# Kernel tuning notes

Measured on AMD Instinct MI355X. Metric: run time of the kernel, lower is better.

Reference implementation:

```python
import jax, jax.numpy as jnp
import numpy as np

B, T, E, H, A, V, C = 4, 256, 256, 256, 256, 32000, 100
NEG = -1e9


def setup_inputs() -> dict:
    key = jax.random.key(0)
    cnt = [0]
    def nk():
        cnt[0] += 1
        return jax.random.fold_in(key, cnt[0])
    def rn(shape, scale=0.05):
        return jax.random.normal(nk(), shape, jnp.float32) * scale
    inp = {
        'input_ids': jax.random.randint(nk(), (B, T), 0, V),
        'category_ids': jax.random.randint(nk(), (B, T), 0, C),
        'emb': rn((V, E)),
        'cat_emb': rn((C, E)),
    }
    in_sizes = [2 * E, H]
    for li, ins in enumerate(in_sizes):
        inp[f'Wih{li}'] = rn((ins, 3 * H)); inp[f'bih{li}'] = rn((3 * H,))
        inp[f'Whh{li}'] = rn((H, 3 * H)); inp[f'bhh{li}'] = rn((3 * H,))
        inp[f'Wh{li}'] = rn((H, A));      inp[f'bh{li}'] = rn((A,))
        inp[f'Wx{li}'] = rn((ins, A));    inp[f'bx{li}'] = rn((A,))
        inp[f'Wth{li}'] = rn((H, A));     inp[f'bth{li}'] = rn((A,))
        inp[f'v{li}'] = rn((A,));         inp[f'bv{li}'] = rn((1,))
    inp['Wctx'] = rn((H + E, 500)); inp['bctx'] = rn((500,))
    inp['Wout'] = rn((500, V));     inp['bout'] = rn((V,))
    return inp


def _cell(x, h, tape, t, Wih, bih, Whh, bhh, Wh, bh, Wx, bx, Wth, bth, v, bv):
    # attention over memory tape positions j < t (tape rows >= t are zeros, masked out)
    att = jnp.tanh(tape @ Wh + bh + (x @ Wx + bx)[:, None, :] + (h @ Wth + bth)[:, None, :])  # [B,T,A]
    scores = att @ v + bv  # [B,T]
    mask = jnp.arange(tape.shape[1]) < t
    scores = jnp.where(mask[None, :], scores, NEG)
    w = jax.nn.softmax(scores, axis=1)
    agg = jnp.einsum('bt,bth->bh', w, tape)
    agg = jnp.where(t > 0, agg, h)  # empty tape at t=0 -> use hidden directly
    gi = x @ Wih + bih
    gh = agg @ Whh + bhh
    ir, iu, inew = jnp.split(gi, 3, axis=1)
    hr, hu, hn = jnp.split(gh, 3, axis=1)
    r = jax.nn.sigmoid(ir + hr)
    u = jax.nn.sigmoid(iu + hu)
    n = jnp.tanh(inew + r * hn)
    return (1.0 - u) * n + u * agg


def _forward(input_ids, category_ids, emb, cat_emb, p0, p1, Wctx, bctx, Wout, bout):
    we = emb[input_ids]          # [B,T,E]
    ce = cat_emb[category_ids]   # [B,T,E]
    x_seq = jnp.concatenate([we, ce], axis=-1)  # [B,T,2E]

    def step(carry, xs):
        h0, h1, tape0, tape1 = carry
        x_t, c_t, t = xs
        # layer 0: category added to both embedding halves
        li0 = jax.nn.relu(x_t + jnp.tile(c_t, (1, 2)))
        nh0 = _cell(li0, h0, tape0, t, *p0)
        tape0 = tape0.at[:, t].set(nh0)
        # layer 1 (dropout is identity in eval)
        li1 = jax.nn.relu(nh0 + c_t)
        nh1 = _cell(li1, h1, tape1, t, *p1)
        tape1 = tape1.at[:, t].set(nh1)
        ctx = jnp.tanh(jnp.concatenate([nh1, c_t], axis=-1) @ Wctx + bctx)
        logits = ctx @ Wout + bout
        return (nh0, nh1, tape0, tape1), logits

    Bn = input_ids.shape[0]
    init = (jnp.zeros((Bn, H), jnp.float32), jnp.zeros((Bn, H), jnp.float32),
            jnp.zeros((Bn, T, H), jnp.float32), jnp.zeros((Bn, T, H), jnp.float32))
    xs = (jnp.swapaxes(x_seq, 0, 1), jnp.swapaxes(ce, 0, 1), jnp.arange(T))
    (h0, h1, _, _), outs = jax.lax.scan(jax.checkpoint(step), init, xs)
    return jnp.swapaxes(outs, 0, 1), h0, h1


def reference(input_ids, category_ids, emb, cat_emb,
              Wih0, bih0, Whh0, bhh0, Wh0, bh0, Wx0, bx0, Wth0, bth0, v0, bv0,
              Wih1, bih1, Whh1, bhh1, Wh1, bh1, Wx1, bx1, Wth1, bth1, v1, bv1,
              Wctx, bctx, Wout, bout):
    p0 = (Wih0, bih0, Whh0, bhh0, Wh0, bh0, Wx0, bx0, Wth0, bth0, v0, bv0)
    p1 = (Wih1, bih1, Whh1, bhh1, Wh1, bh1, Wx1, bx1, Wth1, bth1, v1, bv1)
    return _forward(input_ids, category_ids, emb, cat_emb, p0, p1, Wctx, bctx, Wout, bout)
```

## Files before the change

### kernel.cpp

```cpp
#include <hip/hip_runtime.h>

#define DEVINL __device__ __forceinline__

constexpr int kB = 4, kT = 256, kH = 256, kA = 256, kV = 32000;
constexpr int NBLK = 64;
constexpr int NGRP = 32;
constexpr int NTHR = 512;
constexpr int WSL = 8;
constexpr int SBIAS = 1 << 24;
constexpr int SBIAS_TOT = NGRP * SBIAS;
constexpr unsigned long long CANARY = ~0ull;

typedef __attribute__((ext_vector_type(8))) short bf16x8;
typedef __attribute__((ext_vector_type(4))) float f32x4;

DEVINL float fexp2(float x) { float y; asm("v_exp_f32 %0, %1" : "=v"(y) : "v"(x)); return y; }
DEVINL float frcp(float x)  { float y; asm("v_rcp_f32 %0, %1" : "=v"(y) : "v"(x)); return y; }
DEVINL float f_tanh(float x) {
  float t = fexp2(x * 2.88539008f);
  return 1.f - 2.f * frcp(t + 1.f);
}
DEVINL float f_sig(float x) { return frcp(1.f + fexp2(-x * 1.44269504f)); }

DEVINL float bfu2f(unsigned short u) {
  union { unsigned int i; float f; } c; c.i = ((unsigned int)u) << 16; return c.f;
}
DEVINL unsigned short f2bfu(float f) {
  union { float f; unsigned int i; } c; c.f = f;
  unsigned int r = c.i + 0x7fffu + ((c.i >> 16) & 1u);
  return (unsigned short)(r >> 16);
}
DEVINL unsigned int f2u(float f) { union { float f; unsigned int i; } c; c.f = f; return c.i; }
DEVINL float u2f(unsigned int u) { union { unsigned int i; float f; } c; c.i = u; return c.f; }

DEVINL unsigned long long aload64(const unsigned long long* p) {
  return __hip_atomic_load(p, __ATOMIC_RELAXED, __HIP_MEMORY_SCOPE_AGENT);
}
DEVINL void astore64(unsigned long long* p, unsigned long long v) {
  __hip_atomic_store(p, v, __ATOMIC_RELAXED, __HIP_MEMORY_SCOPE_AGENT);
}

DEVINL bool sready(unsigned long long v) {
  unsigned int lo = (unsigned int)v, hi = (unsigned int)(v >> 32);
  return (((lo + (1u << 23)) >> 24) == (unsigned)NGRP) &&
         (((hi + (1u << 23)) >> 24) == (unsigned)NGRP);
}

DEVINL float dot_bf128(const float* x, const unsigned short* w) {
  float a0 = 0.f, a1 = 0.f, a2 = 0.f, a3 = 0.f;
  float a4 = 0.f, a5 = 0.f, a6 = 0.f, a7 = 0.f;
  const float4*  x4 = (const float4*)x;
  const ushort4* w4 = (const ushort4*)w;
#pragma unroll
  for (int i = 0; i < 32; i += 2) {
    float4 xv0 = x4[i], xv1 = x4[i + 1];
    ushort4 wv0 = w4[i], wv1 = w4[i + 1];
    a0 += xv0.x * bfu2f(wv0.x);
    a1 += xv0.y * bfu2f(wv0.y);
    a2 += xv0.z * bfu2f(wv0.z);
    a3 += xv0.w * bfu2f(wv0.w);
    a4 += xv1.x * bfu2f(wv1.x);
    a5 += xv1.y * bfu2f(wv1.y);
    a6 += xv1.z * bfu2f(wv1.z);
    a7 += xv1.w * bfu2f(wv1.w);
  }
  return ((a0 + a1) + (a2 + a3)) + ((a4 + a5) + (a6 + a7));
}

DEVINL float sc4(const unsigned short* p4p, const float* xp, const float* vr) {
  ushort4 p4 = *(const ushort4*)p4p;
  float accA, accB;
  accA  = f_tanh(bfu2f(p4.x) + xp[0]) * vr[0];
  accB  = f_tanh(bfu2f(p4.y) + xp[1]) * vr[1];
  accA += f_tanh(bfu2f(p4.z) + xp[2]) * vr[2];
  accB += f_tanh(bfu2f(p4.w) + xp[3]) * vr[3];
  return accA + accB;
}

__global__ void init_kernel(int* dst, int nz, int val) {
  for (int i = blockIdx.x * blockDim.x + threadIdx.x; i < nz; i += gridDim.x * blockDim.x)
    dst[i] = val;
}

__global__ void embed_kernel(const int* __restrict__ ids, const int* __restrict__ cids,
                             const float* __restrict__ emb, const float* __restrict__ cat_emb,
                             float* __restrict__ li0_all, float* __restrict__ ce_all,
                             float* __restrict__ cat1_all) {
  int bt = blockIdx.x, e = threadIdx.x;
  int id = ids[bt], cid = cids[bt];
  float we = emb[id * kH + e];
  float ce = cat_emb[cid * kH + e];
  li0_all[bt * 512 + e]       = fmaxf(we + ce, 0.f);
  li0_all[bt * 512 + 256 + e] = fmaxf(ce + ce, 0.f);
  ce_all[bt * 256 + e] = ce;
  cat1_all[bt * 512 + 256 + e] = ce;
}

__global__ __launch_bounds__(256) void gemm_f32(const float* __restrict__ A,
                                                const float* __restrict__ Wm,
                                                const float* __restrict__ bias,
                                                float* __restrict__ C,
                                                int M, int N, int K) {
  __shared__ __align__(16) float As[16][68];
  __shared__ __align__(16) float Bs[16][68];
  int tid = threadIdx.x;
  int tx = tid & 15, ty = tid >> 4;
  int row0 = blockIdx.y * 64, col0 = blockIdx.x * 64;
  int ar = tid >> 2;
  int ak = (tid & 3) * 4;
  int br = tid >> 4;
  int bc = (tid & 15) * 4;
  float acc[4][4] = {};
  for (int k0 = 0; k0 < K; k0 += 16) {
    float4 av = {0.f, 0.f, 0.f, 0.f};
    if (k0 + ak < K) av = *(const float4*)(A + (size_t)(row0 + ar) * K + k0 + ak);
    As[ak + 0][ar] = av.x; As[ak + 1][ar] = av.y; As[ak + 2][ar] = av.z; As[ak + 3][ar] = av.w;
    float4 bv = {0.f, 0.f, 0.f, 0.f};
    int wrow = k0 + br;
    if (wrow < K) {
      if (col0 + bc + 3 < N) bv = *(const float4*)(Wm + (size_t)wrow * N + col0 + bc);
      else {
        float t[4] = {0.f, 0.f, 0.f, 0.f};
        for (int u = 0; u < 4; ++u) if (col0 + bc + u < N) t[u] = Wm[(size_t)wrow * N + col0 + bc + u];
        bv.x = t[0]; bv.y = t[1]; bv.z = t[2]; bv.w = t[3];
      }
    }
    *(float4*)&Bs[br][bc] = bv;
    __syncthreads();
#pragma unroll
    for (int kk = 0; kk < 16; ++kk) {
      float4 a4 = *(const float4*)&As[kk][ty * 4];
      float4 b4 = *(const float4*)&Bs[kk][tx * 4];
      acc[0][0] += a4.x * b4.x; acc[0][1] += a4.x * b4.y; acc[0][2] += a4.x * b4.z; acc[0][3] += a4.x * b4.w;
      acc[1][0] += a4.y * b4.x; acc[1][1] += a4.y * b4.y; acc[1][2] += a4.y * b4.z; acc[1][3] += a4.y * b4.w;
      acc[2][0] += a4.z * b4.x; acc[2][1] += a4.z * b4.y; acc[2][2] += a4.z * b4.z; acc[2][3] += a4.z * b4.w;
      acc[3][0] += a4.w * b4.x; acc[3][1] += a4.w * b4.y; acc[3][2] += a4.w * b4.z; acc[3][3] += a4.w * b4.w;
    }
    __syncthreads();
  }
#pragma unroll
  for (int i = 0; i < 4; ++i) {
    int r = row0 + ty * 4 + i;
#pragma unroll
    for (int j = 0; j < 4; ++j) {
      int c = col0 + tx * 4 + j;
      if (c < N) C[(size_t)r * N + c] = acc[i][j] + bias[c];
    }
  }
}

__global__ __launch_bounds__(256) void gemm_ctx_bf16(const float* __restrict__ A,
                                                     const float* __restrict__ Wm,
                                                     const float* __restrict__ bias,
                                                     unsigned short* __restrict__ Cb) {
  const int N = 500, K = 512;
  __shared__ __align__(16) float As[16][68];
  __shared__ __align__(16) float Bs[16][68];
  int tid = threadIdx.x;
  int tx = tid & 15, ty = tid >> 4;
  int row0 = blockIdx.y * 64, col0 = blockIdx.x * 64;
  int ar = tid >> 2;
  int ak = (tid & 3) * 4;
  int br = tid >> 4;
  int bc = (tid & 15) * 4;
  float acc[4][4] = {};
  for (int k0 = 0; k0 < K; k0 += 16) {
    float4 av = *(const float4*)(A + (size_t)(row0 + ar) * K + k0 + ak);
    As[ak + 0][ar] = av.x; As[ak + 1][ar] = av.y; As[ak + 2][ar] = av.z; As[ak + 3][ar] = av.w;
    float4 bv = {0.f, 0.f, 0.f, 0.f};
    int wrow = k0 + br;
    if (col0 + bc + 3 < N) bv = *(const float4*)(Wm + (size_t)wrow * N + col0 + bc);
    else {
      float t[4] = {0.f, 0.f, 0.f, 0.f};
      for (int u = 0; u < 4; ++u) if (col0 + bc + u < N) t[u] = Wm[(size_t)wrow * N + col0 + bc + u];
      bv.x = t[0]; bv.y = t[1]; bv.z = t[2]; bv.w = t[3];
    }
    *(float4*)&Bs[br][bc] = bv;
    __syncthreads();
#pragma unroll
    for (int kk = 0; kk < 16; ++kk) {
      float4 a4 = *(const float4*)&As[kk][ty * 4];
      float4 b4 = *(const float4*)&Bs[kk][tx * 4];
      acc[0][0] += a4.x * b4.x; acc[0][1] += a4.x * b4.y; acc[0][2] += a4.x * b4.z; acc[0][3] += a4.x * b4.w;
      acc[1][0] += a4.y * b4.x; acc[1][1] += a4.y * b4.y; acc[1][2] += a4.y * b4.z; acc[1][3] += a4.y * b4.w;
      acc[2][0] += a4.z * b4.x; acc[2][1] += a4.z * b4.y; acc[2][2] += a4.z * b4.z; acc[2][3] += a4.z * b4.w;
      acc[3][0] += a4.w * b4.x; acc[3][1] += a4.w * b4.y; acc[3][2] += a4.w * b4.z; acc[3][3] += a4.w * b4.w;
    }
    __syncthreads();
  }
#pragma unroll
  for (int i = 0; i < 4; ++i) {
    int r = row0 + ty * 4 + i;
#pragma unroll
    for (int j = 0; j < 4; ++j) {
      int c = col0 + tx * 4 + j;
      if (c < N) {
        float v = f_tanh(acc[i][j] + bias[c]);
        Cb[(size_t)r * 512 + c] = f2bfu(v);
      } else {
        Cb[(size_t)r * 512 + c] = 0;
      }
    }
  }
}

__global__ __launch_bounds__(256) void gemm_logits_mfma(
    const unsigned short* __restrict__ A,
    const float* __restrict__ Wout,
    const float* __restrict__ bout,
    float* __restrict__ C) {
  __shared__ __align__(16) unsigned short Bt[64][520];
  const int tid = threadIdx.x;
  const int n0 = blockIdx.x * 64;

  for (int idx = tid; idx < 512 * 16; idx += 256) {
    int k = idx >> 4, nq = (idx & 15) << 2;
    if (k < 500) {
      float4 v = *(const float4*)(Wout + (size_t)k * 32000 + n0 + nq);
      Bt[nq + 0][k] = f2bfu(v.x); Bt[nq + 1][k] = f2bfu(v.y);
      Bt[nq + 2][k] = f2bfu(v.z); Bt[nq + 3][k] = f2bfu(v.w);
    } else {
      Bt[nq + 0][k] = 0; Bt[nq + 1][k] = 0; Bt[nq + 2][k] = 0; Bt[nq + 3][k] = 0;
    }
  }
  __syncthreads();

  const int l = tid & 63, w = tid >> 6;
  const int lrow = l & 15, lk = (l >> 4) * 8;
  float bia0 = bout[n0 +  0 + lrow];
  float bia1 = bout[n0 + 16 + lrow];
  float bia2 = bout[n0 + 32 + lrow];
  float bia3 = bout[n0 + 48 + lrow];

  for (int m0 = 0; m0 < 1024; m0 += 64) {
    f32x4 acc0 = {0.f, 0.f, 0.f, 0.f}, acc1 = acc0, acc2 = acc0, acc3 = acc0;
    const unsigned short* Arow = A + (size_t)(m0 + w * 16 + lrow) * 512 + lk;
#pragma unroll
    for (int ks = 0; ks < 16; ++ks) {
      bf16x8 a  = *(const bf16x8*)(Arow + ks * 32);
      bf16x8 b0 = *(const bf16x8*)&Bt[ 0 + lrow][ks * 32 + lk];
      bf16x8 b1 = *(const bf16x8*)&Bt[16 + lrow][ks * 32 + lk];
      bf16x8 b2 = *(const bf16x8*)&Bt[32 + lrow][ks * 32 + lk];
      bf16x8 b3 = *(const bf16x8*)&Bt[48 + lrow][ks * 32 + lk];
      acc0 = __builtin_amdgcn_mfma_f32_16x16x32_bf16(a, b0, acc0, 0, 0, 0);
      acc1 = __builtin_amdgcn_mfma_f32_16x16x32_bf16(a, b1, acc1, 0, 0, 0);
      acc2 = __builtin_amdgcn_mfma_f32_16x16x32_bf16(a, b2, acc2, 0, 0, 0);
      acc3 = __builtin_amdgcn_mfma_f32_16x16x32_bf16(a, b3, acc3, 0, 0, 0);
    }
    int orow = m0 + w * 16 + (l >> 4) * 4;
#pragma unroll
    for (int r = 0; r < 4; ++r) {
      float* Cr = C + (size_t)(orow + r) * 32000 + n0;
      Cr[ 0 + lrow] = acc0[r] + bia0;
      Cr[16 + lrow] = acc1[r] + bia1;
      Cr[32 + lrow] = acc2[r] + bia2;
      Cr[48 + lrow] = acc3[r] + bia3;
    }
  }
}

__global__ __launch_bounds__(NTHR, 1) void coop_kernel(
    const float* __restrict__ gi0_all, const float* __restrict__ xw0_all,
    const float* __restrict__ ce_all,
    unsigned long long* __restrict__ nh0p, unsigned long long* __restrict__ nh1p,
    float* __restrict__ cat1_all, float* __restrict__ out_tail,
    unsigned long long* __restrict__ s0buf, unsigned long long* __restrict__ s1buf,
    const float* __restrict__ Whh0, const float* __restrict__ bhh0,
    const float* __restrict__ Wh0, const float* __restrict__ bh0,
    const float* __restrict__ Wth0, const float* __restrict__ bth0,
    const float* __restrict__ v0,
    const float* __restrict__ Wih1, const float* __restrict__ bih1,
    const float* __restrict__ Whh1, const float* __restrict__ bhh1,
    const float* __restrict__ Wh1, const float* __restrict__ bh1,
    const float* __restrict__ Wx1, const float* __restrict__ bx1,
    const float* __restrict__ Wth1, const float* __restrict__ bth1,
    const float* __restrict__ v1) {
  __shared__ __align__(16) unsigned short tWhh0_s[kT][24][2];
  __shared__ __align__(16) unsigned short tWhh1_s[kT][24][2];
  __shared__ __align__(16) unsigned short tape0_s[kT][16];
  __shared__ __align__(16) unsigned short tape1_s[kT][16];
  __shared__ __align__(16) unsigned short tWh0_s[2][kT][8];
  __shared__ __align__(16) unsigned short tWh1_s[2][kT][8];
  __shared__ __align__(16) unsigned short Wh0c[WSL][264], Wth0c[WSL][264];
  __shared__ __align__(16) unsigned short Wh1c[WSL][264], Wth1c[WSL][264], Wx1c[WSL][264];
  __shared__ __align__(16) unsigned short Whh0c[24][264], Whh1c[24][264], Wih1c[24][264];
  __shared__ float bh0s[8], bth0s[8], bh1s[8], bth1s[8], bx1s[8];
  __shared__ float bhh0s[24], bhh1s[24], bih1s[24];
  __shared__ __align__(16) float nh0_s[2][260], nh1_s[2][260], li1_s[2][260];
  __shared__ __align__(16) float sm_s[4][260];
  __shared__ float xps0_s[2][8], xps1a_s[2][8], xps1b_s[2][8];
  __shared__ float gi1_s[2][24], gh0_s[2][24], gh1_s[2][24];
  __shared__ float agg0_s[2][8], agg1_s[2][8], redsum_s[4][2];
  __shared__ float gipre_s[2][3][8];
  __shared__ float v0s[8], v1s[8];

  const int bid = blockIdx.x, tid = threadIdx.x;
  const int grp = bid >> 5;
  const int bidg = bid & 31;
  const int c0 = bidg * WSL;
  unsigned long long* S0 = s0buf + grp * 768;
  unsigned long long* S1 = s1buf + grp * 768;

  for (int idx = tid; idx < WSL * kH; idx += NTHR) {
    int c = idx >> 8, h = idx & 255, col = c0 + c;
    Wh0c[c][h]  = f2bfu(Wh0[h * kA + col]);
    Wth0c[c][h] = f2bfu(Wth0[h * kA + col]);
    Wh1c[c][h]  = f2bfu(Wh1[h * kA + col]);
    Wth1c[c][h] = f2bfu(Wth1[h * kA + col]);
    Wx1c[c][h]  = f2bfu(Wx1[h * kA + col]);
  }
  for (int idx = tid; idx < 24 * kH; idx += NTHR) {
    int cc = idx >> 8, h = idx & 255;
    int n = (cc >> 3) * kH + c0 + (cc & 7);
    Whh0c[cc][h] = f2bfu(Whh0[h * 768 + n]);
    Whh1c[cc][h] = f2bfu(Whh1[h * 768 + n]);
    Wih1c[cc][h] = f2bfu(Wih1[h * 768 + n]);
  }
  if (tid < 8) {
    int c = c0 + tid;
    bh0s[tid] = bh0[c]; bth0s[tid] = bth0[c];
    bh1s[tid] = bh1[c]; bth1s[tid] = bth1[c]; bx1s[tid] = bx1[c];
    v0s[tid] = v0[c]; v1s[tid] = v1[c];
  }
  if (tid < 24) {
    int n = (tid >> 3) * kH + c0 + (tid & 7);
    bhh0s[tid] = bhh0[n]; bhh1s[tid] = bhh1[n]; bih1s[tid] = bih1[n];
  }
  __syncthreads();

  if (tid < 16) {
    int b = tid & 1, c = tid >> 1, gb = grp * 2 + b;
    const float* gi = gi0_all + (size_t)(gb * kT) * 768;
    int hcol = c0 + c;
    float r = f_sig(gi[hcol] + bhh0s[c]);
    float u = f_sig(gi[256 + hcol] + bhh0s[8 + c]);
    float n = f_tanh(gi[512 + hcol] + r * bhh0s[16 + c]);
    float val = (1.f - u) * n;
    tape0_s[0][c * 2 + b] = f2bfu(val);
    float other = __shfl_xor(val, 2);
    if ((c & 1) == 0) {
      unsigned long long pk = (unsigned long long)f2u(val) |
                              ((unsigned long long)f2u(other) << 32);
      astore64(&nh0p[(size_t)(gb * kT) * 128 + bidg * 4 + (c >> 1)], pk);
    }
  }

  const float SCL = 65536.f;
  const float fxi = 1.44269504f / 65536.f;

  for (int k = 0; k < kT; ++k) {
    {
      int which = tid >> 8;
      int slot = tid & 255;
      int b = slot >> 7, pr = slot & 127, h = pr * 2, gb = grp * 2 + b;
      if (which == 0) {
        const unsigned long long* p = &nh0p[(size_t)(gb * kT + k) * 128 + pr];
        unsigned long long v = aload64(p);
        int it = 0;
        while (v == CANARY) {
          v = aload64(p);
          if (++it > (1 << 24)) break;
        }
        float lo = u2f((unsigned int)v), hi = u2f((unsigned int)(v >> 32));
        nh0_s[b][h] = lo; nh0_s[b][h + 1] = hi;
        float2 ce2 = *(const float2*)&ce_all[(size_t)(gb * kT + k) * 256 + h];
        li1_s[b][h]     = fmaxf(lo + ce2.x, 0.f);
        li1_s[b][h + 1] = fmaxf(hi + ce2.y, 0.f);
      } else if (k > 0) {
        const unsigned long long* p = &nh1p[(size_t)(gb * kT + k - 1) * 128 + pr];
        unsigned long long v = aload64(p);
        int it = 0;
        while (v == CANARY) {
          v = aload64(p);
          if (++it > (1 << 24)) break;
        }
        nh1_s[b][h]     = u2f((unsigned int)v);
        nh1_s[b][h + 1] = u2f((unsigned int)(v >> 32));
      }
    }
    if (tid < 16 && k < kT - 1) {
      int b = tid & 1, c = tid >> 1, gb = grp * 2 + b, hcol = c0 + c;
      const float* gi = gi0_all + (size_t)(gb * kT + k + 1) * 768;
      gipre_s[b][0][c] = gi[hcol];
      gipre_s[b][1][c] = gi[256 + hcol];
      gipre_s[b][2][c] = gi[512 + hcol];
    }
    if (tid >= NTHR - 16) {
      int z = tid - (NTHR - 16);
      int pz = (k + 1) % 3;
      int idx = bidg * 8 + (z & 7);
      if (z < 8) astore64(&S0[pz * 256 + idx], 0ull);
      else       astore64(&S1[pz * 256 + idx], 0ull);
    }
    __syncthreads();

    {
      int p = tid >> 1, half = tid & 1, off = half * 128;
      if (p < 80) {
        if (k < kT - 1) {
          if (p < 16) {
            int b = p & 1, c = p >> 1, gb = grp * 2 + b;
            float xw = xw0_all[(size_t)(gb * kT + k + 1) * kA + c0 + c];
            float acc = dot_bf128(nh0_s[b] + off, Wth0c[c] + off);
            acc += __shfl_xor(acc, 1);
            if (half == 0) xps0_s[b][c] = acc + bth0s[c] + xw;
          } else if (p < 32) {
            int s2 = p - 16; int b = s2 & 1, c = s2 >> 1;
            float acc = dot_bf128(nh0_s[b] + off, Wh0c[c] + off);
            acc += __shfl_xor(acc, 1);
            if (half == 0) tWh0_s[b][k][c] = f2bfu(acc + bh0s[c]);
          } else {
            int s2 = p - 32; int b = s2 & 1, cc = s2 >> 1;
            float acc = dot_bf128(nh0_s[b] + off, Whh0c[cc] + off);
            acc += __shfl_xor(acc, 1);
            if (half == 0) tWhh0_s[k][cc][b] = f2bfu(acc);
          }
        }
      } else if (p < 144) {
        if (p < 96) {
          int s2 = p - 80; int b = s2 & 1, c = s2 >> 1;
          float acc = dot_bf128(li1_s[b] + off, Wx1c[c] + off);
          acc += __shfl_xor(acc, 1);
          if (half == 0) xps1a_s[b][c] = acc + bx1s[c];
        } else {
          int s3 = p - 96; int b = s3 & 1, cc = s3 >> 1;
          float acc = dot_bf128(li1_s[b] + off, Wih1c[cc] + off);
          acc += __shfl_xor(acc, 1);
          if (half == 0) gi1_s[b][cc] = acc + bih1s[cc];
        }
      } else if (p < 224) {
        if (k > 0) {
          if (p < 160) {
            int s2 = p - 144; int b = s2 & 1, c = s2 >> 1;
            float acc = dot_bf128(nh1_s[b] + off, Wth1c[c] + off);
            acc += __shfl_xor(acc, 1);
            if (half == 0) xps1b_s[b][c] = acc + bth1s[c];
          } else if (p < 176) {
            int s3 = p - 160; int b = s3 & 1, c = s3 >> 1;
            float acc = dot_bf128(nh1_s[b] + off, Wh1c[c] + off);
            acc += __shfl_xor(acc, 1);
            if (half == 0) tWh1_s[b][k - 1][c] = f2bfu(acc + bh1s[c]);
          } else {
            int s3 = p - 176; int b = s3 & 1, cc = s3 >> 1;
            float acc = dot_bf128(nh1_s[b] + off, Whh1c[cc] + off);
            acc += __shfl_xor(acc, 1);
            if (half == 0) tWhh1_s[k - 1][cc][b] = f2bfu(acc);
          }
        }
      }
    }
    __syncthreads();

    {
      int cnt0w = k + 1, cnt1w = k;
      int np0 = (k < kT - 1) ? ((cnt0w + 1) >> 1) * 2 : 0;
      int np1 = ((cnt1w + 1) >> 1) * 2;
      int pk = k % 3;
      unsigned long long* d0 = S0 + pk * 256;
      unsigned long long* d1 = S1 + pk * 256;
      for (int pp = tid; pp < np0 + np1; pp += NTHR) {
        float p0, p1; unsigned long long* dst;
        if (pp < np0) {
          int pr = pp >> 1, b = pp & 1, j0 = 2 * pr;
          const float* xp = &xps0_s[b][0];
          p0 = sc4(&tWh0_s[b][j0][0], xp, v0s) + sc4(&tWh0_s[b][j0][4], xp + 4, v0s + 4);
          p1 = 0.f;
          if (j0 + 1 < cnt0w)
            p1 = sc4(&tWh0_s[b][j0 + 1][0], xp, v0s) + sc4(&tWh0_s[b][j0 + 1][4], xp + 4, v0s + 4);
          dst = d0 + b * 128 + pr;
        } else {
          int q = pp - np0; int pr = q >> 1, b = q & 1, j0 = 2 * pr;
          float xp[8];
#pragma unroll
          for (int c = 0; c < 8; ++c) xp[c] = xps1a_s[b][c] + xps1b_s[b][c];
          p0 = sc4(&tWh1_s[b][j0][0], xp, v1s) + sc4(&tWh1_s[b][j0][4], xp + 4, v1s + 4);
          p1 = 0.f;
          if (j0 + 1 < cnt1w)
            p1 = sc4(&tWh1_s[b][j0 + 1][0], xp, v1s) + sc4(&tWh1_s[b][j0 + 1][4], xp + 4, v1s + 4);
          dst = d1 + b * 128 + pr;
        }
        int q0 = (int)rintf(p0 * SCL) + SBIAS;
        int q1 = (int)rintf(p1 * SCL) + SBIAS;
        unsigned long long add = (unsigned long long)(unsigned int)q0 |
                                 ((unsigned long long)(unsigned int)q1 << 32);
        __hip_atomic_fetch_add(dst, add, __ATOMIC_RELAXED, __HIP_MEMORY_SCOPE_AGENT);
      }
    }
    __syncthreads();

    int cnt0 = (k < kT - 1) ? (k + 1) : 0;
    int cnt1 = k;
    {
      int r = tid >> 7, lane = tid & 127;
      float sum = 0.f;
      int cnt = (r < 2) ? cnt0 : cnt1;
      if (cnt) {
        int pk = k % 3;
        const unsigned long long* sb = (r < 2)
            ? S0 + pk * 256 + (r & 1) * 128
            : S1 + pk * 256 + (r & 1) * 128;
        int npr = (cnt + 1) >> 1;
        if (lane < npr) {
          unsigned long long v = aload64(&sb[lane]);
          int it = 0;
          while (!sready(v)) {
            v = aload64(&sb[lane]);
            if (++it > (1 << 24)) break;
          }
          int lo = (int)(unsigned int)(v & 0xffffffffull) - SBIAS_TOT;
          int hi = (int)(unsigned int)(v >> 32) - SBIAS_TOT;
          float e0 = fexp2((float)lo * fxi);
          sm_s[r][2 * lane] = e0; sum += e0;
          if (2 * lane + 1 < cnt) {
            float e1 = fexp2((float)hi * fxi);
            sm_s[r][2 * lane + 1] = e1; sum += e1;
          }
        }
      }
      for (int m = 32; m >= 1; m >>= 1) sum += __shfl_xor(sum, m);
      if ((tid & 63) == 0) redsum_s[r][(tid >> 6) & 1] = sum;
    }
    __syncthreads();

    {
      int slot = tid >> 2, sub = tid & 3;
      float accA = 0.f, accB = 0.f;
      if (slot < 48) {
        if (cnt0) {
          int b = slot & 1, cc = slot >> 1;
#pragma unroll 4
          for (int j = sub; j < cnt0; j += 8) accA += sm_s[b][j] * bfu2f(tWhh0_s[j][cc][b]);
#pragma unroll 4
          for (int j = sub + 4; j < cnt0; j += 8) accB += sm_s[b][j] * bfu2f(tWhh0_s[j][cc][b]);
          float acc = accA + accB;
          acc += __shfl_xor(acc, 1); acc += __shfl_xor(acc, 2);
          if (sub == 0) gh0_s[b][cc] = acc * frcp(redsum_s[b][0] + redsum_s[b][1]) + bhh0s[cc];
        }
      } else if (slot < 64) {
        if (cnt0) {
          int s2 = slot - 48; int b = s2 & 1, c = s2 >> 1;
#pragma unroll 4
          for (int j = sub; j < cnt0; j += 8) accA += sm_s[b][j] * bfu2f(tape0_s[j][c * 2 + b]);
#pragma unroll 4
          for (int j = sub + 4; j < cnt0; j += 8) accB += sm_s[b][j] * bfu2f(tape0_s[j][c * 2 + b]);
          float acc = accA + accB;
          acc += __shfl_xor(acc, 1); acc += __shfl_xor(acc, 2);
          if (sub == 0) agg0_s[b][c] = acc * frcp(redsum_s[b][0] + redsum_s[b][1]);
        }
      } else if (slot < 112) {
        if (cnt1) {
          int s2 = slot - 64; int b = s2 & 1, cc = s2 >> 1;
#pragma unroll 4
          for (int j = sub; j < cnt1; j += 8) accA += sm_s[2 + b][j] * bfu2f(tWhh1_s[j][cc][b]);
#pragma unroll 4
          for (int j = sub + 4; j < cnt1; j += 8) accB += sm_s[2 + b][j] * bfu2f(tWhh1_s[j][cc][b]);
          float acc = accA + accB;
          acc += __shfl_xor(acc, 1); acc += __shfl_xor(acc, 2);
          if (sub == 0) gh1_s[b][cc] = acc * frcp(redsum_s[2 + b][0] + redsum_s[2 + b][1]) + bhh1s[cc];
        }
      } else if (slot < 128) {
        if (cnt1) {
          int s2 = slot - 112; int b = s2 & 1, c = s2 >> 1;
#pragma unroll 4
          for (int j = sub; j < cnt1; j += 8) accA += sm_s[2 + b][j] * bfu2f(tape1_s[j][c * 2 + b]);
#pragma unroll 4
          for (int j = sub + 4; j < cnt1; j += 8) accB += sm_s[2 + b][j] * bfu2f(tape1_s[j][c * 2 + b]);
          float acc = accA + accB;
          acc += __shfl_xor(acc, 1); acc += __shfl_xor(acc, 2);
          if (sub == 0) agg1_s[b][c] = acc * frcp(redsum_s[2 + b][0] + redsum_s[2 + b][1]);
        }
      }
    }
    __syncthreads();

    if (tid < 16) {
      if (k < kT - 1) {
        int b = tid & 1, c = tid >> 1, gb = grp * 2 + b, hcol = c0 + c, t0 = k + 1;
        float agg = agg0_s[b][c];
        float r = f_sig(gipre_s[b][0][c] + gh0_s[b][c]);
        float u = f_sig(gipre_s[b][1][c] + gh0_s[b][8 + c]);
        float n = f_tanh(gipre_s[b][2][c] + r * gh0_s[b][16 + c]);
        float val = (1.f - u) * n + u * agg;
        tape0_s[t0][c * 2 + b] = f2bfu(val);
        if (t0 == kT - 1) out_tail[gb * kH + hcol] = val;
        float other = __shfl_xor(val, 2);
        if ((c & 1) == 0) {
          unsigned long long pk = (unsigned long long)f2u(val) |
                                  ((unsigned long long)f2u(other) << 32);
          astore64(&nh0p[(size_t)(gb * kT + t0) * 128 + bidg * 4 + (c >> 1)], pk);
        }
      }
    } else if (tid >= 64 && tid < 80) {
      int t2 = tid - 64; int b = t2 & 1, c = t2 >> 1, gb = grp * 2 + b, hcol = c0 + c;
      float ghr, ghu, ghn, agg;
      if (k > 0) { ghr = gh1_s[b][c]; ghu = gh1_s[b][8 + c]; ghn = gh1_s[b][16 + c]; agg = agg1_s[b][c]; }
      else       { ghr = bhh1s[c];    ghu = bhh1s[8 + c];    ghn = bhh1s[16 + c];    agg = 0.f; }
      float r = f_sig(gi1_s[b][c] + ghr);
      float u = f_sig(gi1_s[b][8 + c] + ghu);
      float n = f_tanh(gi1_s[b][16 + c] + r * ghn);
      float val = (1.f - u) * n + u * agg;
      tape1_s[k][c * 2 + b] = f2bfu(val);
      cat1_all[(size_t)(gb * kT + k) * 512 + hcol] = val;
      if (k == kT - 1) out_tail[kB * kH + gb * kH + hcol] = val;
      float other = __shfl_xor(val, 2);
      if ((c & 1) == 0) {
        unsigned long long pk = (unsigned long long)f2u(val) |
                                ((unsigned long long)f2u(other) << 32);
        astore64(&nh1p[(size_t)(gb * kT + k) * 128 + bidg * 4 + (c >> 1)], pk);
      }
    }
  }
}

extern "C" void kernel_launch(void* const* d_in, const int* in_sizes, int n_in,
                              void* d_out, int out_size, void* d_ws, size_t ws_size,
                              hipStream_t stream) {
  const int*   input_ids    = (const int*)d_in[0];
  const int*   category_ids = (const int*)d_in[1];
  const float* emb     = (const float*)d_in[2];
  const float* cat_emb = (const float*)d_in[3];
  const float* Wih0 = (const float*)d_in[4];
  const float* bih0 = (const float*)d_in[5];
  const float* Whh0 = (const float*)d_in[6];  const float* bhh0 = (const float*)d_in[7];
  const float* Wh0  = (const float*)d_in[8];  const float* bh0  = (const float*)d_in[9];
  const float* Wx0  = (const float*)d_in[10]; const float* bx0  = (const float*)d_in[11];
  const float* Wth0 = (const float*)d_in[12]; const float* bth0 = (const float*)d_in[13];
  const float* v0   = (const float*)d_in[14];
  const float* Wih1 = (const float*)d_in[16]; const float* bih1 = (const float*)d_in[17];
  const float* Whh1 = (const float*)d_in[18]; const float* bhh1 = (const float*)d_in[19];
  const float* Wh1  = (const float*)d_in[20]; const float* bh1  = (const float*)d_in[21];
  const float* Wx1  = (const float*)d_in[22]; const float* bx1  = (const float*)d_in[23];
  const float* Wth1 = (const float*)d_in[24]; const float* bth1 = (const float*)d_in[25];
  const float* v1   = (const float*)d_in[26];
  const float* Wctx = (const float*)d_in[28]; const float* bctx = (const float*)d_in[29];
  const float* Wout = (const float*)d_in[30]; const float* bout = (const float*)d_in[31];

  float* ws = (float*)d_ws;
  float* li0_all  = ws;
  float* ce_all   = li0_all + 524288;
  float* gi0_all  = ce_all + 262144;
  float* xw0_all  = gi0_all + 786432;
  unsigned long long* nh0p = (unsigned long long*)(xw0_all + 262144);
  unsigned long long* nh1p = nh0p + 131072;
  float* cat1_all = (float*)(nh1p + 131072);
  unsigned short* ctx_bf = (unsigned short*)(cat1_all + 524288);

  unsigned long long* s0buf = (unsigned long long*)li0_all;
  unsigned long long* s1buf = s0buf + 1536;
  int    nzero_s  = 2 * 1536 * 2;
  int    nfill_nh = 2 * 131072 * 2;

  float* out = (float*)d_out;
  float* out_tail = out + (size_t)kB * kT * kV;

  embed_kernel<<<dim3(kB * kT), dim3(256), 0, stream>>>(input_ids, category_ids, emb, cat_emb,
                                                        li0_all, ce_all, cat1_all);
  gemm_f32<<<dim3(12, 16), dim3(256), 0, stream>>>(li0_all, Wih0, bih0, gi0_all, 1024, 768, 512);
  gemm_f32<<<dim3(4, 16), dim3(256), 0, stream>>>(li0_all, Wx0, bx0, xw0_all, 1024, 256, 512);
  init_kernel<<<dim3(8), dim3(512), 0, stream>>>((int*)s0buf, nzero_s, 0);
  init_kernel<<<dim3(128), dim3(512), 0, stream>>>((int*)nh0p, nfill_nh, -1);
  coop_kernel<<<dim3(NBLK), dim3(NTHR), 0, stream>>>(gi0_all, xw0_all, ce_all, nh0p, nh1p,
      cat1_all, out_tail, s0buf, s1buf,
      Whh0, bhh0, Wh0, bh0, Wth0, bth0, v0,
      Wih1, bih1, Whh1, bhh1, Wh1, bh1, Wx1, bx1, Wth1, bth1, v1);
  gemm_ctx_bf16<<<dim3(8, 16), dim3(256), 0, stream>>>(cat1_all, Wctx, bctx, ctx_bf);
  gemm_logits_mfma<<<dim3(500), dim3(256), 0, stream>>>(ctx_bf, Wout, bout, out);
}
```

Before: 2.461 ms.

## Split coop kernel per batch element across 128 blocks instead of 64

Each cooperative block now handles a single batch element instead of two, so the grid doubles to 128 blocks (4 groups of 32). Per-block shared buffers, dot products, the score scratch buffers and the reductions lose their batch dimension. Dot products are split four ways per output with an extra shuffle, and the weighted-sum loops use eight lanes. This shortens the serial per-step critical path inside each block, at the cost of more blocks polling the cross-block sync and each block loading the same weight slices.

Result: faster. 2.072 ms (-15.8%).

```diff
diff --git a/kernel.cpp b/kernel.cpp
--- a/kernel.cpp
+++ b/kernel.cpp
@@ -3,7 +3,7 @@
 #define DEVINL __device__ __forceinline__
 
 constexpr int kB = 4, kT = 256, kH = 256, kA = 256, kV = 32000;
-constexpr int NBLK = 64;
+constexpr int NBLKS = 128;
 constexpr int NGRP = 32;
 constexpr int NTHR = 512;
 constexpr int WSL = 8;
@@ -46,25 +46,19 @@
          (((hi + (1u << 23)) >> 24) == (unsigned)NGRP);
 }
 
-DEVINL float dot_bf128(const float* x, const unsigned short* w) {
+DEVINL float dot_bf64(const float* x, const unsigned short* w) {
   float a0 = 0.f, a1 = 0.f, a2 = 0.f, a3 = 0.f;
-  float a4 = 0.f, a5 = 0.f, a6 = 0.f, a7 = 0.f;
   const float4*  x4 = (const float4*)x;
   const ushort4* w4 = (const ushort4*)w;
 #pragma unroll
-  for (int i = 0; i < 32; i += 2) {
-    float4 xv0 = x4[i], xv1 = x4[i + 1];
-    ushort4 wv0 = w4[i], wv1 = w4[i + 1];
-    a0 += xv0.x * bfu2f(wv0.x);
-    a1 += xv0.y * bfu2f(wv0.y);
-    a2 += xv0.z * bfu2f(wv0.z);
-    a3 += xv0.w * bfu2f(wv0.w);
-    a4 += xv1.x * bfu2f(wv1.x);
-    a5 += xv1.y * bfu2f(wv1.y);
-    a6 += xv1.z * bfu2f(wv1.z);
-    a7 += xv1.w * bfu2f(wv1.w);
-  }
-  return ((a0 + a1) + (a2 + a3)) + ((a4 + a5) + (a6 + a7));
+  for (int i = 0; i < 16; ++i) {
+    float4 xv = x4[i]; ushort4 wv = w4[i];
+    a0 += xv.x * bfu2f(wv.x);
+    a1 += xv.y * bfu2f(wv.y);
+    a2 += xv.z * bfu2f(wv.z);
+    a3 += xv.w * bfu2f(wv.w);
+  }
+  return (a0 + a1) + (a2 + a3);
 }
 
 DEVINL float sc4(const unsigned short* p4p, const float* xp, const float* vr) {
@@ -275,31 +269,32 @@
     const float* __restrict__ Wx1, const float* __restrict__ bx1,
     const float* __restrict__ Wth1, const float* __restrict__ bth1,
     const float* __restrict__ v1) {
-  __shared__ __align__(16) unsigned short tWhh0_s[kT][24][2];
-  __shared__ __align__(16) unsigned short tWhh1_s[kT][24][2];
-  __shared__ __align__(16) unsigned short tape0_s[kT][16];
-  __shared__ __align__(16) unsigned short tape1_s[kT][16];
-  __shared__ __align__(16) unsigned short tWh0_s[2][kT][8];
-  __shared__ __align__(16) unsigned short tWh1_s[2][kT][8];
+  __shared__ __align__(16) unsigned short tWhh0_s[kT][24];
+  __shared__ __align__(16) unsigned short tWhh1_s[kT][24];
+  __shared__ __align__(16) unsigned short tape0_s[kT][8];
+  __shared__ __align__(16) unsigned short tape1_s[kT][8];
+  __shared__ __align__(16) unsigned short tWh0_s[kT][8];
+  __shared__ __align__(16) unsigned short tWh1_s[kT][8];
   __shared__ __align__(16) unsigned short Wh0c[WSL][264], Wth0c[WSL][264];
   __shared__ __align__(16) unsigned short Wh1c[WSL][264], Wth1c[WSL][264], Wx1c[WSL][264];
   __shared__ __align__(16) unsigned short Whh0c[24][264], Whh1c[24][264], Wih1c[24][264];
   __shared__ float bh0s[8], bth0s[8], bh1s[8], bth1s[8], bx1s[8];
   __shared__ float bhh0s[24], bhh1s[24], bih1s[24];
-  __shared__ __align__(16) float nh0_s[2][260], nh1_s[2][260], li1_s[2][260];
-  __shared__ __align__(16) float sm_s[4][260];
-  __shared__ float xps0_s[2][8], xps1a_s[2][8], xps1b_s[2][8];
-  __shared__ float gi1_s[2][24], gh0_s[2][24], gh1_s[2][24];
-  __shared__ float agg0_s[2][8], agg1_s[2][8], redsum_s[4][2];
-  __shared__ float gipre_s[2][3][8];
+  __shared__ __align__(16) float nh0_s[260], nh1_s[260], li1_s[260];
+  __shared__ __align__(16) float sm_s[2][260];
+  __shared__ float xps0_s[8], xps1a_s[8], xps1b_s[8];
+  __shared__ float gi1_s[24], gh0_s[24], gh1_s[24];
+  __shared__ float agg0_s[8], agg1_s[8], redsum_s[2][2];
+  __shared__ float gipre_s[3][8];
   __shared__ float v0s[8], v1s[8];
 
   const int bid = blockIdx.x, tid = threadIdx.x;
   const int grp = bid >> 5;
   const int bidg = bid & 31;
   const int c0 = bidg * WSL;
-  unsigned long long* S0 = s0buf + grp * 768;
-  unsigned long long* S1 = s1buf + grp * 768;
+  const int gb = grp;
+  unsigned long long* S0 = s0buf + grp * 384;
+  unsigned long long* S1 = s1buf + grp * 384;
 
   for (int idx = tid; idx < WSL * kH; idx += NTHR) {
     int c = idx >> 8, h = idx & 255, col = c0 + c;
@@ -328,16 +323,15 @@
   }
   __syncthreads();
 
-  if (tid < 16) {
-    int b = tid & 1, c = tid >> 1, gb = grp * 2 + b;
+  if (tid < 8) {
+    int c = tid, hcol = c0 + c;
     const float* gi = gi0_all + (size_t)(gb * kT) * 768;
-    int hcol = c0 + c;
     float r = f_sig(gi[hcol] + bhh0s[c]);
     float u = f_sig(gi[256 + hcol] + bhh0s[8 + c]);
     float n = f_tanh(gi[512 + hcol] + r * bhh0s[16 + c]);
     float val = (1.f - u) * n;
-    tape0_s[0][c * 2 + b] = f2bfu(val);
-    float other = __shfl_xor(val, 2);
+    tape0_s[0][c] = f2bfu(val);
+    float other = __shfl_xor(val, 1);
     if ((c & 1) == 0) {
       unsigned long long pk = (unsigned long long)f2u(val) |
                               ((unsigned long long)f2u(other) << 32);
@@ -349,10 +343,9 @@
   const float fxi = 1.44269504f / 65536.f;
 
   for (int k = 0; k < kT; ++k) {
-    {
-      int which = tid >> 8;
-      int slot = tid & 255;
-      int b = slot >> 7, pr = slot & 127, h = pr * 2, gb = grp * 2 + b;
+    if (tid < 256) {
+      int which = tid >> 7;
+      int pr = tid & 127, h = pr * 2;
       if (which == 0) {
         const unsigned long long* p = &nh0p[(size_t)(gb * kT + k) * 128 + pr];
         unsigned long long v = aload64(p);
@@ -362,10 +355,10 @@
           if (++it > (1 << 24)) break;
         }
         float lo = u2f((unsigned int)v), hi = u2f((unsigned int)(v >> 32));
-        nh0_s[b][h] = lo; nh0_s[b][h + 1] = hi;
+        nh0_s[h] = lo; nh0_s[h + 1] = hi;
         float2 ce2 = *(const float2*)&ce_all[(size_t)(gb * kT + k) * 256 + h];
-        li1_s[b][h]     = fmaxf(lo + ce2.x, 0.f);
-        li1_s[b][h + 1] = fmaxf(hi + ce2.y, 0.f);
+        li1_s[h]     = fmaxf(lo + ce2.x, 0.f);
+        li1_s[h + 1] = fmaxf(hi + ce2.y, 0.f);
       } else if (k > 0) {
         const unsigned long long* p = &nh1p[(size_t)(gb * kT + k - 1) * 128 + pr];
         unsigned long long v = aload64(p);
@@ -374,77 +367,79 @@
           v = aload64(p);
           if (++it > (1 << 24)) break;
         }
-        nh1_s[b][h]     = u2f((unsigned int)v);
-        nh1_s[b][h + 1] = u2f((unsigned int)(v >> 32));
-      }
-    }
-    if (tid < 16 && k < kT - 1) {
-      int b = tid & 1, c = tid >> 1, gb = grp * 2 + b, hcol = c0 + c;
+        nh1_s[h]     = u2f((unsigned int)v);
+        nh1_s[h + 1] = u2f((unsigned int)(v >> 32));
+      }
+    }
+    if (tid >= 256 && tid < 264 && k < kT - 1) {
+      int c = tid - 256, hcol = c0 + c;
       const float* gi = gi0_all + (size_t)(gb * kT + k + 1) * 768;
-      gipre_s[b][0][c] = gi[hcol];
-      gipre_s[b][1][c] = gi[256 + hcol];
-      gipre_s[b][2][c] = gi[512 + hcol];
-    }
-    if (tid >= NTHR - 16) {
-      int z = tid - (NTHR - 16);
+      gipre_s[0][c] = gi[hcol];
+      gipre_s[1][c] = gi[256 + hcol];
+      gipre_s[2][c] = gi[512 + hcol];
+    }
+    if (tid >= NTHR - 8) {
+      int z = tid - (NTHR - 8);
       int pz = (k + 1) % 3;
-      int idx = bidg * 8 + (z & 7);
-      if (z < 8) astore64(&S0[pz * 256 + idx], 0ull);
-      else       astore64(&S1[pz * 256 + idx], 0ull);
+      int idx = bidg * 4 + (z & 3);
+      if (z < 4) astore64(&S0[pz * 128 + idx], 0ull);
+      else       astore64(&S1[pz * 128 + idx], 0ull);
     }
     __syncthreads();
 
     {
-      int p = tid >> 1, half = tid & 1, off = half * 128;
-      if (p < 80) {
+      int p = tid >> 2, q = tid & 3, off = q * 64;
+      if (p < 40) {
         if (k < kT - 1) {
-          if (p < 16) {
-            int b = p & 1, c = p >> 1, gb = grp * 2 + b;
-            float xw = xw0_all[(size_t)(gb * kT + k + 1) * kA + c0 + c];
-            float acc = dot_bf128(nh0_s[b] + off, Wth0c[c] + off);
-            acc += __shfl_xor(acc, 1);
-            if (half == 0) xps0_s[b][c] = acc + bth0s[c] + xw;
-          } else if (p < 32) {
-            int s2 = p - 16; int b = s2 & 1, c = s2 >> 1;
-            float acc = dot_bf128(nh0_s[b] + off, Wh0c[c] + off);
-            acc += __shfl_xor(acc, 1);
-            if (half == 0) tWh0_s[b][k][c] = f2bfu(acc + bh0s[c]);
+          if (p < 8) {
+            int c = p;
+            float acc = dot_bf64(nh0_s + off, Wth0c[c] + off);
+            acc += __shfl_xor(acc, 1); acc += __shfl_xor(acc, 2);
+            if (q == 0) {
+              float xw = xw0_all[(size_t)(gb * kT + k + 1) * kA + c0 + c];
+              xps0_s[c] = acc + bth0s[c] + xw;
+            }
+          } else if (p < 16) {
+            int c = p - 8;
+            float acc = dot_bf64(nh0_s + off, Wh0c[c] + off);
+            acc += __shfl_xor(acc, 1); acc += __shfl_xor(acc, 2);
+            if (q == 0) tWh0_s[k][c] = f2bfu(acc + bh0s[c]);
           } else {
-            int s2 = p - 32; int b = s2 & 1, cc = s2 >> 1;
-            float acc = dot_bf128(nh0_s[b] + off, Whh0c[cc] + off);
-            acc += __shfl_xor(acc, 1);
-            if (half == 0) tWhh0_s[k][cc][b] = f2bfu(acc);
+            int cc = p - 16;
+            float acc = dot_bf64(nh0_s + off, Whh0c[cc] + off);
+            acc += __shfl_xor(acc, 1); acc += __shfl_xor(acc, 2);
+            if (q == 0) tWhh0_s[k][cc] = f2bfu(acc);
           }
         }
-      } else if (p < 144) {
-        if (p < 96) {
-          int s2 = p - 80; int b = s2 & 1, c = s2 >> 1;
-          float acc = dot_bf128(li1_s[b] + off, Wx1c[c] + off);
-          acc += __shfl_xor(acc, 1);
-          if (half == 0) xps1a_s[b][c] = acc + bx1s[c];
+      } else if (p < 72) {
+        if (p < 64) {
+          int cc = p - 40;
+          float acc = dot_bf64(li1_s + off, Wih1c[cc] + off);
+          acc += __shfl_xor(acc, 1); acc += __shfl_xor(acc, 2);
+          if (q == 0) gi1_s[cc] = acc + bih1s[cc];
         } else {
-          int s3 = p - 96; int b = s3 & 1, cc = s3 >> 1;
-          float acc = dot_bf128(li1_s[b] + off, Wih1c[cc] + off);
-          acc += __shfl_xor(acc, 1);
-          if (half == 0) gi1_s[b][cc] = acc + bih1s[cc];
-        }
-      } else if (p < 224) {
+          int c = p - 64;
+          float acc = dot_bf64(li1_s + off, Wx1c[c] + off);
+          acc += __shfl_xor(acc, 1); acc += __shfl_xor(acc, 2);
+          if (q == 0) xps1a_s[c] = acc + bx1s[c];
+        }
+      } else if (p < 112) {
         if (k > 0) {
-          if (p < 160) {
-            int s2 = p - 144; int b = s2 & 1, c = s2 >> 1;
-            float acc = dot_bf128(nh1_s[b] + off, Wth1c[c] + off);
-            acc += __shfl_xor(acc, 1);
-            if (half == 0) xps1b_s[b][c] = acc + bth1s[c];
-          } else if (p < 176) {
-            int s3 = p - 160; int b = s3 & 1, c = s3 >> 1;
-            float acc = dot_bf128(nh1_s[b] + off, Wh1c[c] + off);
-            acc += __shfl_xor(acc, 1);
-            if (half == 0) tWh1_s[b][k - 1][c] = f2bfu(acc + bh1s[c]);
+          if (p < 80) {
+            int c = p - 72;
+            float acc = dot_bf64(nh1_s + off, Wth1c[c] + off);
+            acc += __shfl_xor(acc, 1); acc += __shfl_xor(acc, 2);
+            if (q == 0) xps1b_s[c] = acc + bth1s[c];
+          } else if (p < 88) {
+            int c = p - 80;
+            float acc = dot_bf64(nh1_s + off, Wh1c[c] + off);
+            acc += __shfl_xor(acc, 1); acc += __shfl_xor(acc, 2);
+            if (q == 0) tWh1_s[k - 1][c] = f2bfu(acc + bh1s[c]);
           } else {
-            int s3 = p - 176; int b = s3 & 1, cc = s3 >> 1;
-            float acc = dot_bf128(nh1_s[b] + off, Whh1c[cc] + off);
-            acc += __shfl_xor(acc, 1);
-            if (half == 0) tWhh1_s[k - 1][cc][b] = f2bfu(acc);
+            int cc = p - 88;
+            float acc = dot_bf64(nh1_s + off, Whh1c[cc] + off);
+            acc += __shfl_xor(acc, 1); acc += __shfl_xor(acc, 2);
+            if (q == 0) tWhh1_s[k - 1][cc] = f2bfu(acc);
           }
         }
       }
@@ -453,31 +448,30 @@
 
     {
       int cnt0w = k + 1, cnt1w = k;
-      int np0 = (k < kT - 1) ? ((cnt0w + 1) >> 1) * 2 : 0;
-      int np1 = ((cnt1w + 1) >> 1) * 2;
+      int np0 = (k < kT - 1) ? ((cnt0w + 1) >> 1) : 0;
+      int np1 = (cnt1w + 1) >> 1;
       int pk = k % 3;
-      unsigned long long* d0 = S0 + pk * 256;
-      unsigned long long* d1 = S1 + pk * 256;
+      unsigned long long* d0 = S0 + pk * 128;
+      unsigned long long* d1 = S1 + pk * 128;
       for (int pp = tid; pp < np0 + np1; pp += NTHR) {
         float p0, p1; unsigned long long* dst;
         if (pp < np0) {
-          int pr = pp >> 1, b = pp & 1, j0 = 2 * pr;
-          const float* xp = &xps0_s[b][0];
-          p0 = sc4(&tWh0_s[b][j0][0], xp, v0s) + sc4(&tWh0_s[b][j0][4], xp + 4, v0s + 4);
+          int j0 = 2 * pp;
+          p0 = sc4(&tWh0_s[j0][0], xps0_s, v0s) + sc4(&tWh0_s[j0][4], xps0_s + 4, v0s + 4);
           p1 = 0.f;
           if (j0 + 1 < cnt0w)
-            p1 = sc4(&tWh0_s[b][j0 + 1][0], xp, v0s) + sc4(&tWh0_s[b][j0 + 1][4], xp + 4, v0s + 4);
-          dst = d0 + b * 128 + pr;
+            p1 = sc4(&tWh0_s[j0 + 1][0], xps0_s, v0s) + sc4(&tWh0_s[j0 + 1][4], xps0_s + 4, v0s + 4);
+          dst = d0 + pp;
         } else {
-          int q = pp - np0; int pr = q >> 1, b = q & 1, j0 = 2 * pr;
+          int pr = pp - np0, j0 = 2 * pr;
           float xp[8];
 #pragma unroll
-          for (int c = 0; c < 8; ++c) xp[c] = xps1a_s[b][c] + xps1b_s[b][c];
-          p0 = sc4(&tWh1_s[b][j0][0], xp, v1s) + sc4(&tWh1_s[b][j0][4], xp + 4, v1s + 4);
+          for (int c = 0; c < 8; ++c) xp[c] = xps1a_s[c] + xps1b_s[c];
+          p0 = sc4(&tWh1_s[j0][0], xp, v1s) + sc4(&tWh1_s[j0][4], xp + 4, v1s + 4);
           p1 = 0.f;
           if (j0 + 1 < cnt1w)
-            p1 = sc4(&tWh1_s[b][j0 + 1][0], xp, v1s) + sc4(&tWh1_s[b][j0 + 1][4], xp + 4, v1s + 4);
-          dst = d1 + b * 128 + pr;
+            p1 = sc4(&tWh1_s[j0 + 1][0], xp, v1s) + sc4(&tWh1_s[j0 + 1][4], xp + 4, v1s + 4);
+          dst = d1 + pr;
         }
         int q0 = (int)rintf(p0 * SCL) + SBIAS;
         int q1 = (int)rintf(p1 * SCL) + SBIAS;
@@ -490,15 +484,13 @@
 
     int cnt0 = (k < kT - 1) ? (k + 1) : 0;
     int cnt1 = k;
-    {
+    if (tid < 256) {
       int r = tid >> 7, lane = tid & 127;
       float sum = 0.f;
-      int cnt = (r < 2) ? cnt0 : cnt1;
+      int cnt = (r == 0) ? cnt0 : cnt1;
       if (cnt) {
         int pk = k % 3;
-        const unsigned long long* sb = (r < 2)
-            ? S0 + pk * 256 + (r & 1) * 128
-            : S1 + pk * 256 + (r & 1) * 128;
+        const unsigned long long* sb = (r == 0) ? S0 + pk * 128 : S1 + pk * 128;
         int npr = (cnt + 1) >> 1;
         if (lane < npr) {
           unsigned long long v = aload64(&sb[lane]);
@@ -523,86 +515,86 @@
     __syncthreads();
 
     {
-      int slot = tid >> 2, sub = tid & 3;
+      int slot = tid >> 3, sub = tid & 7;
       float accA = 0.f, accB = 0.f;
-      if (slot < 48) {
+      if (slot < 24) {
         if (cnt0) {
-          int b = slot & 1, cc = slot >> 1;
-#pragma unroll 4
-          for (int j = sub; j < cnt0; j += 8) accA += sm_s[b][j] * bfu2f(tWhh0_s[j][cc][b]);
-#pragma unroll 4
-          for (int j = sub + 4; j < cnt0; j += 8) accB += sm_s[b][j] * bfu2f(tWhh0_s[j][cc][b]);
+          int cc = slot;
+#pragma unroll 4
+          for (int j = sub; j < cnt0; j += 16) accA += sm_s[0][j] * bfu2f(tWhh0_s[j][cc]);
+#pragma unroll 4
+          for (int j = sub + 8; j < cnt0; j += 16) accB += sm_s[0][j] * bfu2f(tWhh0_s[j][cc]);
           float acc = accA + accB;
-          acc += __shfl_xor(acc, 1); acc += __shfl_xor(acc, 2);
-          if (sub == 0) gh0_s[b][cc] = acc * frcp(redsum_s[b][0] + redsum_s[b][1]) + bhh0s[cc];
+          acc += __shfl_xor(acc, 1); acc += __shfl_xor(acc, 2); acc += __shfl_xor(acc, 4);
+          if (sub == 0) gh0_s[cc] = acc * frcp(redsum_s[0][0] + redsum_s[0][1]) + bhh0s[cc];
+        }
+      } else if (slot < 32) {
+        if (cnt0) {
+          int c = slot - 24;
+#pragma unroll 4
+          for (int j = sub; j < cnt0; j += 16) accA += sm_s[0][j] * bfu2f(tape0_s[j][c]);
+#pragma unroll 4
+          for (int j = sub + 8; j < cnt0; j += 16) accB += sm_s[0][j] * bfu2f(tape0_s[j][c]);
+          float acc = accA + accB;
+          acc += __shfl_xor(acc, 1); acc += __shfl_xor(acc, 2); acc += __shfl_xor(acc, 4);
+          if (sub == 0) agg0_s[c] = acc * frcp(redsum_s[0][0] + redsum_s[0][1]);
+        }
+      } else if (slot < 56) {
+        if (cnt1) {
+          int cc = slot - 32;
+#pragma unroll 4
+          for (int j = sub; j < cnt1; j += 16) accA += sm_s[1][j] * bfu2f(tWhh1_s[j][cc]);
+#pragma unroll 4
+          for (int j = sub + 8; j < cnt1; j += 16) accB += sm_s[1][j] * bfu2f(tWhh1_s[j][cc]);
+          float acc = accA + accB;
+          acc += __shfl_xor(acc, 1); acc += __shfl_xor(acc, 2); acc += __shfl_xor(acc, 4);
+          if (sub == 0) gh1_s[cc] = acc * frcp(redsum_s[1][0] + redsum_s[1][1]) + bhh1s[cc];
         }
       } else if (slot < 64) {
-        if (cnt0) {
-          int s2 = slot - 48; int b = s2 & 1, c = s2 >> 1;
-#pragma unroll 4
-          for (int j = sub; j < cnt0; j += 8) accA += sm_s[b][j] * bfu2f(tape0_s[j][c * 2 + b]);
-#pragma unroll 4
-          for (int j = sub + 4; j < cnt0; j += 8) accB += sm_s[b][j] * bfu2f(tape0_s[j][c * 2 + b]);
+        if (cnt1) {
+          int c = slot - 56;
+#pragma unroll 4
+          for (int j = sub; j < cnt1; j += 16) accA += sm_s[1][j] * bfu2f(tape1_s[j][c]);
+#pragma unroll 4
+          for (int j = sub + 8; j < cnt1; j += 16) accB += sm_s[1][j] * bfu2f(tape1_s[j][c]);
           float acc = accA + accB;
-          acc += __shfl_xor(acc, 1); acc += __shfl_xor(acc, 2);
-          if (sub == 0) agg0_s[b][c] = acc * frcp(redsum_s[b][0] + redsum_s[b][1]);
-        }
-      } else if (slot < 112) {
-        if (cnt1) {
-          int s2 = slot - 64; int b = s2 & 1, cc = s2 >> 1;
-#pragma unroll 4
-          for (int j = sub; j < cnt1; j += 8) accA += sm_s[2 + b][j] * bfu2f(tWhh1_s[j][cc][b]);
-#pragma unroll 4
-          for (int j = sub + 4; j < cnt1; j += 8) accB += sm_s[2 + b][j] * bfu2f(tWhh1_s[j][cc][b]);
-          float acc = accA + accB;
-          acc += __shfl_xor(acc, 1); acc += __shfl_xor(acc, 2);
-          if (sub == 0) gh1_s[b][cc] = acc * frcp(redsum_s[2 + b][0] + redsum_s[2 + b][1]) + bhh1s[cc];
-        }
-      } else if (slot < 128) {
-        if (cnt1) {
-          int s2 = slot - 112; int b = s2 & 1, c = s2 >> 1;
-#pragma unroll 4
-          for (int j = sub; j < cnt1; j += 8) accA += sm_s[2 + b][j] * bfu2f(tape1_s[j][c * 2 + b]);
-#pragma unroll 4
-          for (int j = sub + 4; j < cnt1; j += 8) accB += sm_s[2 + b][j] * bfu2f(tape1_s[j][c * 2 + b]);
-          float acc = accA + accB;
-          acc += __shfl_xor(acc, 1); acc += __shfl_xor(acc, 2);
-          if (sub == 0) agg1_s[b][c] = acc * frcp(redsum_s[2 + b][0] + redsum_s[2 + b][1]);
-        }
-      }
-    }
-    __syncthreads();
-
-    if (tid < 16) {
+          acc += __shfl_xor(acc, 1); acc += __shfl_xor(acc, 2); acc += __shfl_xor(acc, 4);
+          if (sub == 0) agg1_s[c] = acc * frcp(redsum_s[1][0] + redsum_s[1][1]);
+        }
+      }
+    }
+    __syncthreads();
+
+    if (tid < 8) {
       if (k < kT - 1) {
-        int b = tid & 1, c = tid >> 1, gb = grp * 2 + b, hcol = c0 + c, t0 = k + 1;
-        float agg = agg0_s[b][c];
-        float r = f_sig(gipre_s[b][0][c] + gh0_s[b][c]);
-        float u = f_sig(gipre_s[b][1][c] + gh0_s[b][8 + c]);
-        float n = f_tanh(gipre_s[b][2][c] + r * gh0_s[b][16 + c]);
+        int c = tid, hcol = c0 + c, t0 = k + 1;
+        float agg = agg0_s[c];
+        float r = f_sig(gipre_s[0][c] + gh0_s[c]);
+        float u = f_sig(gipre_s[1][c] + gh0_s[8 + c]);
+        float n = f_tanh(gipre_s[2][c] + r * gh0_s[16 + c]);
         float val = (1.f - u) * n + u * agg;
-        tape0_s[t0][c * 2 + b] = f2bfu(val);
+        tape0_s[t0][c] = f2bfu(val);
         if (t0 == kT - 1) out_tail[gb * kH + hcol] = val;
-        float other = __shfl_xor(val, 2);
+        float other = __shfl_xor(val, 1);
         if ((c & 1) == 0) {
           unsigned long long pk = (unsigned long long)f2u(val) |
                                   ((unsigned long long)f2u(other) << 32);
           astore64(&nh0p[(size_t)(gb * kT + t0) * 128 + bidg * 4 + (c >> 1)], pk);
         }
       }
-    } else if (tid >= 64 && tid < 80) {
-      int t2 = tid - 64; int b = t2 & 1, c = t2 >> 1, gb = grp * 2 + b, hcol = c0 + c;
+    } else if (tid >= 64 && tid < 72) {
+      int c = tid - 64, hcol = c0 + c;
       float ghr, ghu, ghn, agg;
-      if (k > 0) { ghr = gh1_s[b][c]; ghu = gh1_s[b][8 + c]; ghn = gh1_s[b][16 + c]; agg = agg1_s[b][c]; }
-      else       { ghr = bhh1s[c];    ghu = bhh1s[8 + c];    ghn = bhh1s[16 + c];    agg = 0.f; }
-      float r = f_sig(gi1_s[b][c] + ghr);
-      float u = f_sig(gi1_s[b][8 + c] + ghu);
-      float n = f_tanh(gi1_s[b][16 + c] + r * ghn);
+      if (k > 0) { ghr = gh1_s[c]; ghu = gh1_s[8 + c]; ghn = gh1_s[16 + c]; agg = agg1_s[c]; }
+      else       { ghr = bhh1s[c]; ghu = bhh1s[8 + c]; ghn = bhh1s[16 + c]; agg = 0.f; }
+      float r = f_sig(gi1_s[c] + ghr);
+      float u = f_sig(gi1_s[8 + c] + ghu);
+      float n = f_tanh(gi1_s[16 + c] + r * ghn);
       float val = (1.f - u) * n + u * agg;
-      tape1_s[k][c * 2 + b] = f2bfu(val);
+      tape1_s[k][c] = f2bfu(val);
       cat1_all[(size_t)(gb * kT + k) * 512 + hcol] = val;
       if (k == kT - 1) out_tail[kB * kH + gb * kH + hcol] = val;
-      float other = __shfl_xor(val, 2);
+      float other = __shfl_xor(val, 1);
       if ((c & 1) == 0) {
         unsigned long long pk = (unsigned long long)f2u(val) |
                                 ((unsigned long long)f2u(other) << 32);
@@ -659,7 +651,7 @@
   gemm_f32<<<dim3(4, 16), dim3(256), 0, stream>>>(li0_all, Wx0, bx0, xw0_all, 1024, 256, 512);
   init_kernel<<<dim3(8), dim3(512), 0, stream>>>((int*)s0buf, nzero_s, 0);
   init_kernel<<<dim3(128), dim3(512), 0, stream>>>((int*)nh0p, nfill_nh, -1);
-  coop_kernel<<<dim3(NBLK), dim3(NTHR), 0, stream>>>(gi0_all, xw0_all, ce_all, nh0p, nh1p,
+  coop_kernel<<<dim3(NBLKS), dim3(NTHR), 0, stream>>>(gi0_all, xw0_all, ce_all, nh0p, nh1p,
       cat1_all, out_tail, s0buf, s1buf,
       Whh0, bhh0, Wh0, bh0, Wth0, bth0, v0,
       Wih1, bih1, Whh1, bhh1, Wh1, bh1, Wx1, bx1, Wth1, bth1, v1);
```
